# Kernel tuning notes

Hardware: AMD Instinct MI355X
Metric: run time of the kernel (lower is better)

The kernel has to match this reference:

```python
import jax, jax.numpy as jnp
import numpy as np

B, S, E = 8, 2048, 2048

def setup_inputs() -> dict:
    key = jax.random.key(0)
    k1, k2, k3, k4 = jax.random.split(key, 4)
    return {
        "batch_size": B,
        "seq_len": S,
        "embedding_dim": E,
        "time_decay": jax.random.normal(k1, (E,), dtype=jnp.float32),
        "time_first": jax.random.normal(k2, (E,), dtype=jnp.float32),
        "k": jax.random.normal(k3, (B, S, E), dtype=jnp.float32),
        "v": jax.random.normal(k4, (B, S, E), dtype=jnp.float32),
    }

def _wkv(time_decay, time_first, k, v):
    dtype = k.dtype
    b, s, e = k.shape
    # time-major for scan: [S, B, E]
    k_t = jnp.transpose(k, (1, 0, 2))
    v_t = jnp.transpose(v, (1, 0, 2))
    tf = time_first[None, :]  # [1, E] broadcast over batch
    td = time_decay[None, :]
    aa0 = jnp.zeros((b, e), dtype=dtype)
    bb0 = jnp.zeros((b, e), dtype=dtype)
    eps0 = jnp.zeros((b, e), dtype=dtype)  # MIN_VAL = 0.0

    def step(carry, kv):
        aa, bb, eps = carry
        kt, vt = kv
        e_tf_k = jnp.exp(tf + kt - eps)
        y_t = (aa + vt * e_tf_k) / (bb + e_tf_k)
        eps_next = jnp.maximum(td + eps, kt)
        e_td_k = jnp.exp(td + eps - eps_next)
        e_k = jnp.exp(kt - eps_next)
        aa = aa * e_td_k + vt * e_k
        bb = bb * e_td_k + e_k
        return (aa, bb, eps_next), y_t

    _, y_t = jax.lax.scan(step, (aa0, bb0, eps0), (k_t, v_t))
    return jnp.transpose(y_t, (1, 0, 2))  # [B, S, E]

def reference(batch_size, seq_len, embedding_dim, time_decay, time_first, k, v):
    return _wkv(time_decay, time_first, k, v)
```

## Files before the change

kernel.cpp:

```cpp
#include <hip/hip_runtime.h>


#define B_ 8
#define S_ 2048
#define E_ 2048
constexpr int BE = B_ * E_;
constexpr int CH = 16;
constexpr int CL = S_ / CH;

__global__ __launch_bounds__(64) void wkv_pass1(
    const float* __restrict__ td_g,
    const float* __restrict__ k_g, const float* __restrict__ v_g,
    float* __restrict__ sa, float* __restrict__ sb, float* __restrict__ se)
{
    const int gid = blockIdx.x * 64 + threadIdx.x;
    const int j = gid >> 14;
    const int c = gid & (BE - 1);
    const int b = c >> 11;
    const int e = c & (E_ - 1);
    const float td = td_g[e];
    const long base = (long)b * S_ * E_ + (long)(j * CL) * E_ + e;
    const float* __restrict__ kp = k_g + base;
    const float* __restrict__ vp = v_g + base;

    float aa = 0.f, bb = 0.f, eps = 0.f;
    constexpr int U = 8;
    float kA[U], vA[U], kB[U], vB[U];
#pragma unroll
    for (int i = 0; i < U; ++i) { kA[i] = kp[i * E_]; vA[i] = vp[i * E_]; }

    auto st = [&](float kt, float vt) {
        const float tde = td + eps;
        const float m   = fmaxf(tde, kt);
        const float p   = __expf(tde - m);
        const float q   = __expf(kt - m);
        aa = fmaf(aa, p, vt * q);
        bb = fmaf(bb, p, q);
        eps = m;
    };

    for (int t0 = 0; t0 < CL; t0 += 2 * U) {
#pragma unroll
        for (int i = 0; i < U; ++i) { kB[i] = kp[(t0 + U + i) * E_]; vB[i] = vp[(t0 + U + i) * E_]; }
#pragma unroll
        for (int i = 0; i < U; ++i) st(kA[i], vA[i]);
        if (t0 + 2 * U < CL) {
#pragma unroll
            for (int i = 0; i < U; ++i) { kA[i] = kp[(t0 + 2*U + i) * E_]; vA[i] = vp[(t0 + 2*U + i) * E_]; }
        }
#pragma unroll
        for (int i = 0; i < U; ++i) st(kB[i], vB[i]);
    }
    sa[j * BE + c] = aa;
    sb[j * BE + c] = bb;
    se[j * BE + c] = eps;
}

__global__ __launch_bounds__(64) void wkv_pass2(
    const float* __restrict__ td_g,
    const float* __restrict__ sa, const float* __restrict__ sb, const float* __restrict__ se,
    float* __restrict__ ia, float* __restrict__ ib, float* __restrict__ ie)
{
    const int c = blockIdx.x * 64 + threadIdx.x;
    const int e = c & (E_ - 1);
    const float Ltd = (float)CL * td_g[e];

    float aa = 0.f, bb = 0.f, eps = 0.f;
    ia[c] = 0.f; ib[c] = 0.f; ie[c] = 0.f;
#pragma unroll
    for (int j = 1; j < CH; ++j) {
        const float a_c = sa[(j - 1) * BE + c];
        const float b_c = sb[(j - 1) * BE + c];
        const float e_c = se[(j - 1) * BE + c];
        const float ed  = eps + Ltd;
        const float ne  = fmaxf(ed, e_c);
        const float f1  = __expf(ed - ne);
        const float f2  = __expf(e_c - ne);
        aa = aa * f1 + a_c * f2;
        bb = bb * f1 + b_c * f2;
        eps = ne;
        ia[j * BE + c] = aa;
        ib[j * BE + c] = bb;
        ie[j * BE + c] = eps;
    }
}

__global__ __launch_bounds__(64) void wkv_pass3(
    const float* __restrict__ td_g, const float* __restrict__ tf_g,
    const float* __restrict__ k_g, const float* __restrict__ v_g,
    const float* __restrict__ ia, const float* __restrict__ ib, const float* __restrict__ ie,
    float* __restrict__ y_g)
{
    const int gid = blockIdx.x * 64 + threadIdx.x;
    const int j = gid >> 14;
    const int c = gid & (BE - 1);
    const int b = c >> 11;
    const int e = c & (E_ - 1);
    const float td = td_g[e];
    const float tf = tf_g[e];
    const long base = (long)b * S_ * E_ + (long)(j * CL) * E_ + e;
    const float* __restrict__ kp = k_g + base;
    const float* __restrict__ vp = v_g + base;
    float* __restrict__ yp = y_g + base;

    float aa = ia[j * BE + c];
    float bb = ib[j * BE + c];
    float eps = ie[j * BE + c];

    constexpr int U = 8;
    float kA[U], vA[U], kB[U], vB[U];
#pragma unroll
    for (int i = 0; i < U; ++i) { kA[i] = kp[i * E_]; vA[i] = vp[i * E_]; }

    auto st = [&](float kt, float vt, int t) {
        const float e1 = __expf(tf + kt - eps);
        const float y  = __fdividef(fmaf(vt, e1, aa), bb + e1);
        __builtin_nontemporal_store(y, &yp[t * E_]);
        const float tde = td + eps;
        const float m   = fmaxf(tde, kt);
        const float p   = __expf(tde - m);
        const float q   = __expf(kt - m);
        aa = fmaf(aa, p, vt * q);
        bb = fmaf(bb, p, q);
        eps = m;
    };

    for (int t0 = 0; t0 < CL; t0 += 2 * U) {
#pragma unroll
        for (int i = 0; i < U; ++i) { kB[i] = kp[(t0 + U + i) * E_]; vB[i] = vp[(t0 + U + i) * E_]; }
#pragma unroll
        for (int i = 0; i < U; ++i) st(kA[i], vA[i], t0 + i);
        if (t0 + 2 * U < CL) {
#pragma unroll
            for (int i = 0; i < U; ++i) { kA[i] = kp[(t0 + 2*U + i) * E_]; vA[i] = vp[(t0 + 2*U + i) * E_]; }
        }
#pragma unroll
        for (int i = 0; i < U; ++i) st(kB[i], vB[i], t0 + U + i);
    }
}

__global__ __launch_bounds__(64) void wkv_single(
    const float* __restrict__ td_g, const float* __restrict__ tf_g,
    const float* __restrict__ k_g, const float* __restrict__ v_g,
    float* __restrict__ y_g)
{
    const int c = blockIdx.x * 64 + threadIdx.x;
    const int b = c >> 11;
    const int e = c & (E_ - 1);
    const float td = td_g[e];
    const float tf = tf_g[e];
    const long base = (long)b * S_ * E_ + e;
    const float* __restrict__ kp = k_g + base;
    const float* __restrict__ vp = v_g + base;
    float* __restrict__ yp = y_g + base;
    float aa = 0.f, bb = 0.f, eps = 0.f;
    for (int t = 0; t < S_; ++t) {
        const float kt = kp[t * E_], vt = vp[t * E_];
        const float e1 = __expf(tf + kt - eps);
        yp[t * E_] = __fdividef(fmaf(vt, e1, aa), bb + e1);
        const float tde = td + eps;
        const float m = fmaxf(tde, kt);
        const float p = __expf(tde - m);
        const float q = __expf(kt - m);
        aa = fmaf(aa, p, vt * q);
        bb = fmaf(bb, p, q);
        eps = m;
    }
}

extern "C" void kernel_launch(void* const* d_in, const int* in_sizes, int n_in,
                              void* d_out, int out_size, void* d_ws, size_t ws_size,
                              hipStream_t stream) {
    const float* td = (const float*)d_in[3];
    const float* tf = (const float*)d_in[4];
    const float* k  = (const float*)d_in[5];
    const float* v  = (const float*)d_in[6];
    float* y        = (float*)d_out;
    (void)in_sizes; (void)n_in; (void)out_size;

    const size_t arr = (size_t)CH * BE * sizeof(float);
    if (ws_size < 6 * arr) {
        hipLaunchKernelGGL(wkv_single, dim3(BE / 64), dim3(64), 0, stream, td, tf, k, v, y);
        return;
    }
    float* sa = (float*)d_ws;
    float* sb = sa + CH * BE;
    float* se = sb + CH * BE;
    float* ia = se + CH * BE;
    float* ib = ia + CH * BE;
    float* ie = ib + CH * BE;

    hipLaunchKernelGGL(wkv_pass1, dim3((CH - 1) * BE / 64), dim3(64), 0, stream,
                       td, k, v, sa, sb, se);
    hipLaunchKernelGGL(wkv_pass2, dim3(BE / 64), dim3(64), 0, stream,
                       td, sa, sb, se, ia, ib, ie);
    hipLaunchKernelGGL(wkv_pass3, dim3(CH * BE / 64), dim3(64), 0, stream,
                       td, tf, k, v, ia, ib, ie, y);
}
```

Before: 372.9 us.

## Vectorize WKV scan passes with float4 channels and double chunk count

Each thread in pass1 and pass3 now handles four adjacent channels through float4 loads and stores instead of one scalar channel. The chunk count goes from 16 to 32, and block size goes from 64 to 256. The aim is wider, more efficient memory transactions while keeping enough parallel threads, since vectorization cuts the thread count by four. The cost is four times the registers per thread for the unrolled prefetch buffers and a larger workspace for chunk states. The pass2 carry scan also grows longer.

```diff
diff --git a/kernel.cpp b/kernel.cpp
--- a/kernel.cpp
+++ b/kernel.cpp
@@ -4,64 +4,68 @@
 #define B_ 8
 #define S_ 2048
 #define E_ 2048
-constexpr int BE = B_ * E_;
-constexpr int CH = 16;
-constexpr int CL = S_ / CH;
-
-__global__ __launch_bounds__(64) void wkv_pass1(
+constexpr int BE  = B_ * E_;
+constexpr int CH  = 32;
+constexpr int CL  = S_ / CH;
+constexpr int NT4 = BE / 4;
+constexpr int E4  = E_ / 4;
+
+typedef float f32x4 __attribute__((ext_vector_type(4)));
+
+__global__ __launch_bounds__(256) void wkv_pass1(
     const float* __restrict__ td_g,
     const float* __restrict__ k_g, const float* __restrict__ v_g,
     float* __restrict__ sa, float* __restrict__ sb, float* __restrict__ se)
 {
-    const int gid = blockIdx.x * 64 + threadIdx.x;
-    const int j = gid >> 14;
-    const int c = gid & (BE - 1);
-    const int b = c >> 11;
-    const int e = c & (E_ - 1);
-    const float td = td_g[e];
-    const long base = (long)b * S_ * E_ + (long)(j * CL) * E_ + e;
-    const float* __restrict__ kp = k_g + base;
-    const float* __restrict__ vp = v_g + base;
-
-    float aa = 0.f, bb = 0.f, eps = 0.f;
+    const int gid = blockIdx.x * 256 + threadIdx.x;
+    const int j  = gid >> 12;
+    const int c4 = gid & (NT4 - 1);
+    const int b  = c4 >> 9;
+    const int e4 = c4 & (E4 - 1);
+    const float4 td4 = ((const float4*)td_g)[e4];
+    const long base4 = ((long)b * S_ * E_ + (long)(j * CL) * E_) / 4 + e4;
+    const float4* __restrict__ kp = (const float4*)k_g + base4;
+    const float4* __restrict__ vp = (const float4*)v_g + base4;
+
+    float4 aa = {0,0,0,0}, bb = {0,0,0,0}, eps = {0,0,0,0};
     constexpr int U = 8;
-    float kA[U], vA[U], kB[U], vB[U];
-#pragma unroll
-    for (int i = 0; i < U; ++i) { kA[i] = kp[i * E_]; vA[i] = vp[i * E_]; }
-
-    auto st = [&](float kt, float vt) {
-        const float tde = td + eps;
-        const float m   = fmaxf(tde, kt);
-        const float p   = __expf(tde - m);
-        const float q   = __expf(kt - m);
-        aa = fmaf(aa, p, vt * q);
-        bb = fmaf(bb, p, q);
-        eps = m;
-    };
+    float4 kA[U], vA[U], kB[U], vB[U];
+#pragma unroll
+    for (int i = 0; i < U; ++i) { kA[i] = kp[i * E4]; vA[i] = vp[i * E4]; }
+
+#define STEP1(k4, v4, C) { \
+    const float tde = td4.C + eps.C; \
+    const float m   = fmaxf(tde, (k4).C); \
+    const float p   = __expf(tde - m); \
+    const float q   = __expf((k4).C - m); \
+    aa.C = fmaf(aa.C, p, (v4).C * q); \
+    bb.C = fmaf(bb.C, p, q); \
+    eps.C = m; }
+#define STEP1ALL(k4, v4) { STEP1(k4,v4,x) STEP1(k4,v4,y) STEP1(k4,v4,z) STEP1(k4,v4,w) }
 
     for (int t0 = 0; t0 < CL; t0 += 2 * U) {
 #pragma unroll
-        for (int i = 0; i < U; ++i) { kB[i] = kp[(t0 + U + i) * E_]; vB[i] = vp[(t0 + U + i) * E_]; }
-#pragma unroll
-        for (int i = 0; i < U; ++i) st(kA[i], vA[i]);
+        for (int i = 0; i < U; ++i) { kB[i] = kp[(t0+U+i) * E4]; vB[i] = vp[(t0+U+i) * E4]; }
+#pragma unroll
+        for (int i = 0; i < U; ++i) STEP1ALL(kA[i], vA[i]);
         if (t0 + 2 * U < CL) {
 #pragma unroll
-            for (int i = 0; i < U; ++i) { kA[i] = kp[(t0 + 2*U + i) * E_]; vA[i] = vp[(t0 + 2*U + i) * E_]; }
+            for (int i = 0; i < U; ++i) { kA[i] = kp[(t0+2*U+i) * E4]; vA[i] = vp[(t0+2*U+i) * E4]; }
         }
 #pragma unroll
-        for (int i = 0; i < U; ++i) st(kB[i], vB[i]);
-    }
-    sa[j * BE + c] = aa;
-    sb[j * BE + c] = bb;
-    se[j * BE + c] = eps;
-}
-
-__global__ __launch_bounds__(64) void wkv_pass2(
+        for (int i = 0; i < U; ++i) STEP1ALL(kB[i], vB[i]);
+    }
+    ((float4*)sa)[j * NT4 + c4] = aa;
+    ((float4*)sb)[j * NT4 + c4] = bb;
+    ((float4*)se)[j * NT4 + c4] = eps;
+}
+
+__global__ __launch_bounds__(256) void wkv_pass2(
     const float* __restrict__ td_g,
     const float* __restrict__ sa, const float* __restrict__ sb, const float* __restrict__ se,
     float* __restrict__ ia, float* __restrict__ ib, float* __restrict__ ie)
 {
-    const int c = blockIdx.x * 64 + threadIdx.x;
+    const int c = blockIdx.x * 256 + threadIdx.x;
     const int e = c & (E_ - 1);
     const float Ltd = (float)CL * td_g[e];
 
@@ -85,57 +89,58 @@
     }
 }
 
-__global__ __launch_bounds__(64) void wkv_pass3(
+__global__ __launch_bounds__(256) void wkv_pass3(
     const float* __restrict__ td_g, const float* __restrict__ tf_g,
     const float* __restrict__ k_g, const float* __restrict__ v_g,
     const float* __restrict__ ia, const float* __restrict__ ib, const float* __restrict__ ie,
     float* __restrict__ y_g)
 {
-    const int gid = blockIdx.x * 64 + threadIdx.x;
-    const int j = gid >> 14;
-    const int c = gid & (BE - 1);
-    const int b = c >> 11;
-    const int e = c & (E_ - 1);
-    const float td = td_g[e];
-    const float tf = tf_g[e];
-    const long base = (long)b * S_ * E_ + (long)(j * CL) * E_ + e;
-    const float* __restrict__ kp = k_g + base;
-    const float* __restrict__ vp = v_g + base;
-    float* __restrict__ yp = y_g + base;
-
-    float aa = ia[j * BE + c];
-    float bb = ib[j * BE + c];
-    float eps = ie[j * BE + c];
+    const int gid = blockIdx.x * 256 + threadIdx.x;
+    const int j  = gid >> 12;
+    const int c4 = gid & (NT4 - 1);
+    const int b  = c4 >> 9;
+    const int e4 = c4 & (E4 - 1);
+    const float4 td4 = ((const float4*)td_g)[e4];
+    const float4 tf4 = ((const float4*)tf_g)[e4];
+    const long base4 = ((long)b * S_ * E_ + (long)(j * CL) * E_) / 4 + e4;
+    const float4* __restrict__ kp = (const float4*)k_g + base4;
+    const float4* __restrict__ vp = (const float4*)v_g + base4;
+    f32x4* __restrict__ yp = (f32x4*)y_g + base4;
+
+    float4 aa  = ((const float4*)ia)[j * NT4 + c4];
+    float4 bb  = ((const float4*)ib)[j * NT4 + c4];
+    float4 eps = ((const float4*)ie)[j * NT4 + c4];
 
     constexpr int U = 8;
-    float kA[U], vA[U], kB[U], vB[U];
-#pragma unroll
-    for (int i = 0; i < U; ++i) { kA[i] = kp[i * E_]; vA[i] = vp[i * E_]; }
-
-    auto st = [&](float kt, float vt, int t) {
-        const float e1 = __expf(tf + kt - eps);
-        const float y  = __fdividef(fmaf(vt, e1, aa), bb + e1);
-        __builtin_nontemporal_store(y, &yp[t * E_]);
-        const float tde = td + eps;
-        const float m   = fmaxf(tde, kt);
-        const float p   = __expf(tde - m);
-        const float q   = __expf(kt - m);
-        aa = fmaf(aa, p, vt * q);
-        bb = fmaf(bb, p, q);
-        eps = m;
-    };
+    float4 kA[U], vA[U], kB[U], vB[U];
+#pragma unroll
+    for (int i = 0; i < U; ++i) { kA[i] = kp[i * E4]; vA[i] = vp[i * E4]; }
+
+#define STEP3(k4, v4, C, YI) { \
+    const float e1 = __expf(tf4.C + (k4).C - eps.C); \
+    y4[YI] = __fdividef(fmaf((v4).C, e1, aa.C), bb.C + e1); \
+    const float tde = td4.C + eps.C; \
+    const float m   = fmaxf(tde, (k4).C); \
+    const float p   = __expf(tde - m); \
+    const float q   = __expf((k4).C - m); \
+    aa.C = fmaf(aa.C, p, (v4).C * q); \
+    bb.C = fmaf(bb.C, p, q); \
+    eps.C = m; }
+#define STEP3ALL(k4, v4, t) { f32x4 y4; \
+    STEP3(k4,v4,x,0) STEP3(k4,v4,y,1) STEP3(k4,v4,z,2) STEP3(k4,v4,w,3) \
+    __builtin_nontemporal_store(y4, &yp[(t) * E4]); }
 
     for (int t0 = 0; t0 < CL; t0 += 2 * U) {
 #pragma unroll
-        for (int i = 0; i < U; ++i) { kB[i] = kp[(t0 + U + i) * E_]; vB[i] = vp[(t0 + U + i) * E_]; }
-#pragma unroll
-        for (int i = 0; i < U; ++i) st(kA[i], vA[i], t0 + i);
+        for (int i = 0; i < U; ++i) { kB[i] = kp[(t0+U+i) * E4]; vB[i] = vp[(t0+U+i) * E4]; }
+#pragma unroll
+        for (int i = 0; i < U; ++i) STEP3ALL(kA[i], vA[i], t0 + i);
         if (t0 + 2 * U < CL) {
 #pragma unroll
-            for (int i = 0; i < U; ++i) { kA[i] = kp[(t0 + 2*U + i) * E_]; vA[i] = vp[(t0 + 2*U + i) * E_]; }
+            for (int i = 0; i < U; ++i) { kA[i] = kp[(t0+2*U+i) * E4]; vA[i] = vp[(t0+2*U+i) * E4]; }
         }
 #pragma unroll
-        for (int i = 0; i < U; ++i) st(kB[i], vB[i], t0 + U + i);
+        for (int i = 0; i < U; ++i) STEP3ALL(kB[i], vB[i], t0 + U + i);
     }
 }
 
@@ -190,10 +195,10 @@
     float* ib = ia + CH * BE;
     float* ie = ib + CH * BE;
 
-    hipLaunchKernelGGL(wkv_pass1, dim3((CH - 1) * BE / 64), dim3(64), 0, stream,
+    hipLaunchKernelGGL(wkv_pass1, dim3((CH - 1) * NT4 / 256), dim3(256), 0, stream,
                        td, k, v, sa, sb, se);
-    hipLaunchKernelGGL(wkv_pass2, dim3(BE / 64), dim3(64), 0, stream,
+    hipLaunchKernelGGL(wkv_pass2, dim3(BE / 256), dim3(256), 0, stream,
                        td, sa, sb, se, ia, ib, ie);
-    hipLaunchKernelGGL(wkv_pass3, dim3(CH * BE / 64), dim3(64), 0, stream,
+    hipLaunchKernelGGL(wkv_pass3, dim3(CH * NT4 / 256), dim3(256), 0, stream,
                        td, tf, k, v, ia, ib, ie, y);
 }
```

After: 379.6 us. Within noise of the previous version (+1.8%).
